# Optimization experiments

Hardware: AMD Instinct MI355X
Metric: run time of the kernel (lower is better)

The kernel has to match this reference:

```python
import jax, jax.numpy as jnp
import numpy as np
import math

E = 1024      # hidden_dim = embed_dim (num_heads=1 so head_dim=E)
ND = 512      # output_dim = asymmetric value dim
N_DOMAIN = 2048
LN_EPS = 1e-5
SCALE = math.sqrt(1.0 / E) * 2.0 * math.log(N_DOMAIN)


def layernorm(x, g, b):
    mu = jnp.mean(x, axis=-1, keepdims=True)
    var = jnp.var(x, axis=-1, keepdims=True)
    return (x - mu) * jax.lax.rsqrt(var + LN_EPS) * g + b


def setup_inputs() -> dict:
    key = jax.random.key(0)
    ks = jax.random.split(key, 5)
    B, L = 8, 2048
    return {
        "x": jax.random.normal(ks[0], (B, L, E), dtype=jnp.float32),
        "in_proj_w": jax.random.normal(ks[1], (2 * E + ND, E), dtype=jnp.float32) * 0.02,
        "w1": jax.random.normal(ks[2], (2048, ND), dtype=jnp.float32) * 0.02,
        "b1": jnp.zeros((2048,), dtype=jnp.float32),
        "w2": jax.random.normal(ks[3], (ND, 2048), dtype=jnp.float32) * 0.02,
        "b2": jnp.zeros((ND,), dtype=jnp.float32),
        "g1": jnp.ones((ND,), dtype=jnp.float32),
        "be1": jnp.zeros((ND,), dtype=jnp.float32),
        "g2": jnp.ones((ND,), dtype=jnp.float32),
        "be2": jnp.zeros((ND,), dtype=jnp.float32),
    }


def reference(x, in_proj_w, w1, b1, w2, b2, g1, be1, g2, be2):
    # fused in-projection (no bias): q,k get E dims, v gets ND dims
    proj = jnp.einsum("ble,fe->blf", x, in_proj_w)
    q = proj[..., :E]
    k = proj[..., E:2 * E]
    v = proj[..., 2 * E:]
    # custom scale: sqrt(1/head_dim) * 2 * log(N)
    scores = jnp.einsum("bld,bsd->bls", q * SCALE, k)  # [B, L, S]
    attn_w = jax.nn.softmax(scores, axis=-1)
    attn_out = jnp.einsum("bls,bsd->bld", attn_w, v)   # [B, L, ND] (no out proj)
    # skip=False (hidden_dim != output_dim): norm1(attn) only
    h = layernorm(attn_out, g1, be1)
    ff = jnp.einsum("bld,fd->blf", h, w1) + b1
    ff = jnp.einsum("blf,df->bld", jax.nn.relu(ff), w2) + b2
    return layernorm(h + ff, g2, be2)
```

## Files before the change

kernel.cpp:

```cpp
#include <hip/hip_runtime.h>
#include <hip/hip_bf16.h>

typedef unsigned short u16;
typedef unsigned int u32;
typedef float f32x4 __attribute__((ext_vector_type(4)));
typedef _Float16 f16x8 __attribute__((ext_vector_type(8)));
typedef u32 u32x4 __attribute__((ext_vector_type(4)));
typedef u32 u32x2 __attribute__((ext_vector_type(2)));

#define SEQ 2048
#define EDIM 1024

__device__ __forceinline__ u16 f2h(float f) {
  _Float16 h = (_Float16)f;
  return __builtin_bit_cast(u16, h);
}
__device__ __forceinline__ float h2f(u16 u) {
  return (float)__builtin_bit_cast(_Float16, u);
}
__device__ __forceinline__ u32 pk(float a, float b) {
  return (u32)f2h(a) | ((u32)f2h(b) << 16);
}

__global__ __launch_bounds__(256) void cvt_f16(const float* __restrict__ in,
                                               u16* __restrict__ out, int n8) {
  int i = blockIdx.x * 256 + threadIdx.x;
  if (i >= n8) return;
  const f32x4* p = (const f32x4*)(in + (size_t)i * 8);
  f32x4 a = p[0], b = p[1];
  u32x4 o = {pk(a[0], a[1]), pk(a[2], a[3]), pk(b[0], b[1]), pk(b[2], b[3])};
  *(u32x4*)(out + (size_t)i * 8) = o;
}

struct GemmP {
  const u16* A; const u16* B;
  int lda, ldb, K;
  long bsA, bsB, bsC;
  float* Cf;
  int ldc;
  u16* Cb;
  const float* bias;
  const u16* resid;
  u16* qk; u16* vT;
  float scale;
};

template <int EPI>
__global__ __launch_bounds__(256) void gemm_bt(GemmP p) {
  __shared__ __align__(16) char lds[32768];
  const int tid = threadIdx.x;
  const int lane = tid & 63;
  const int wave = tid >> 6;
  const int wm = wave >> 1, wn = wave & 1;
  const int bn0 = blockIdx.x * 128;
  const int bm0 = blockIdx.y * 128;
  const int z = blockIdx.z;

  const u16* gA[4]; const u16* gB[4];
  int ldsA[4], ldsB[4];
  {
    const u16* Ab = p.A + (long)z * p.bsA + (long)bm0 * p.lda;
    const u16* Bb = p.B + (long)z * p.bsB + (long)bn0 * p.ldb;
#pragma unroll
    for (int i = 0; i < 4; ++i) {
      int ch = i * 256 + tid;
      int row = ch >> 3, s = ch & 7;
      int ks = ((s ^ (row & 7)) << 3);
      gA[i] = Ab + (long)row * p.lda + ks;
      gB[i] = Bb + (long)row * p.ldb + ks;
      ldsA[i] = ch * 16;
      ldsB[i] = 16384 + ch * 16;
    }
  }
  auto stage = [&]() {
#pragma unroll
    for (int i = 0; i < 4; ++i) {
      __builtin_amdgcn_global_load_lds(
          (const __attribute__((address_space(1))) u32*)gA[i],
          (__attribute__((address_space(3))) u32*)(lds + ldsA[i]), 16, 0, 0);
      gA[i] += 64;
    }
#pragma unroll
    for (int i = 0; i < 4; ++i) {
      __builtin_amdgcn_global_load_lds(
          (const __attribute__((address_space(1))) u32*)gB[i],
          (__attribute__((address_space(3))) u32*)(lds + ldsB[i]), 16, 0, 0);
      gB[i] += 64;
    }
  };

  int ao[2][4], bo[2][4];
#pragma unroll
  for (int h = 0; h < 2; ++h) {
#pragma unroll
    for (int i = 0; i < 4; ++i) {
      int rA = wm * 64 + i * 16 + (lane & 15);
      ao[h][i] = rA * 128 + ((((h << 2) | (lane >> 4)) ^ (rA & 7)) << 4);
      int rB = wn * 64 + i * 16 + (lane & 15);
      bo[h][i] = 16384 + rB * 128 + ((((h << 2) | (lane >> 4)) ^ (rB & 7)) << 4);
    }
  }

  f32x4 acc[4][4] = {};
  stage();
  const int nk = p.K >> 6;
  for (int kt = 0; kt < nk; ++kt) {
    __syncthreads();
#pragma unroll
    for (int h = 0; h < 2; ++h) {
      f16x8 av[4], bv[4];
#pragma unroll
      for (int i = 0; i < 4; ++i) av[i] = *(const f16x8*)(lds + ao[h][i]);
#pragma unroll
      for (int j = 0; j < 4; ++j) bv[j] = *(const f16x8*)(lds + bo[h][j]);
#pragma unroll
      for (int i = 0; i < 4; ++i)
#pragma unroll
        for (int j = 0; j < 4; ++j)
          acc[i][j] = __builtin_amdgcn_mfma_f32_16x16x32_f16(av[i], bv[j], acc[i][j], 0, 0, 0);
    }
    __syncthreads();
    if (kt + 1 < nk) stage();
  }

#pragma unroll
  for (int i = 0; i < 4; ++i) {
#pragma unroll
    for (int j = 0; j < 4; ++j) {
      int mb = bm0 + wm * 64 + i * 16 + ((lane >> 4) << 2);
      int n = bn0 + wn * 64 + j * 16 + (lane & 15);
      if constexpr (EPI == 1) {
        int b = mb >> 11, l0 = mb & 2047;
        if (n < EDIM) {
          u16* dst = p.qk + (long)b * 4194304 + (long)l0 * 1024 + n;
#pragma unroll
          for (int r = 0; r < 4; ++r) dst[r * 1024] = f2h(acc[i][j][r] * p.scale);
        } else if (n < 2 * EDIM) {
          u16* dst = p.qk + (long)b * 4194304 + 2097152 + (long)l0 * 1024 + (n - EDIM);
#pragma unroll
          for (int r = 0; r < 4; ++r) dst[r * 1024] = f2h(acc[i][j][r]);
        } else {
          u16* dst = p.vT + (long)b * 1048576 + (long)(n - 2 * EDIM) * 2048 + l0;
          u32x2 w = {pk(acc[i][j][0], acc[i][j][1]), pk(acc[i][j][2], acc[i][j][3])};
          *(u32x2*)dst = w;
        }
      } else if constexpr (EPI == 2) {
        u16* dst = p.Cb + (long)mb * p.ldc + n;
        float bias = p.bias[n];
#pragma unroll
        for (int r = 0; r < 4; ++r) dst[(long)r * p.ldc] = f2h(fmaxf(acc[i][j][r] + bias, 0.f));
      } else if constexpr (EPI == 3) {
        float bias = p.bias[n];
        float* dst = p.Cf + (long)mb * 512 + n;
        const u16* rs = p.resid + (long)mb * 512 + n;
#pragma unroll
        for (int r = 0; r < 4; ++r) dst[r * 512] = acc[i][j][r] + bias + h2f(rs[r * 512]);
      } else {
        u16* dst = p.Cb + (long)z * p.bsC + (long)mb * p.ldc + n;
#pragma unroll
        for (int r = 0; r < 4; ++r) dst[(long)r * p.ldc] = f2h(acc[i][j][r]);
      }
    }
  }
}

__global__ __launch_bounds__(256) void softmax_rows(const u16* __restrict__ S,
                                                    u16* __restrict__ W, int b0) {
  int r = blockIdx.x;
  int z = r >> 11, l = r & 2047;
  int tid = threadIdx.x, lane = tid & 63, wv = tid >> 6;
  const u16* x = S + (long)r * 2048 + tid * 8;
  u32x4 raw = *(const u32x4*)x;
  float e[8];
#pragma unroll
  for (int q = 0; q < 4; ++q) {
    e[2 * q] = h2f((u16)(raw[q] & 0xffff));
    e[2 * q + 1] = h2f((u16)(raw[q] >> 16));
  }
  float m = e[0];
#pragma unroll
  for (int q = 1; q < 8; ++q) m = fmaxf(m, e[q]);
#pragma unroll
  for (int off = 32; off; off >>= 1) m = fmaxf(m, __shfl_xor(m, off));
  __shared__ float red[8];
  if (lane == 0) red[wv] = m;
  __syncthreads();
  m = fmaxf(fmaxf(red[0], red[1]), fmaxf(red[2], red[3]));
  float s = 0.f;
#pragma unroll
  for (int q = 0; q < 8; ++q) { e[q] = __expf(e[q] - m); s += e[q]; }
#pragma unroll
  for (int off = 32; off; off >>= 1) s += __shfl_xor(s, off);
  if (lane == 0) red[4 + wv] = s;
  __syncthreads();
  s = red[4] + red[5] + red[6] + red[7];
  float inv = 1.f / s;
  u32x4 o = {pk(e[0] * inv, e[1] * inv), pk(e[2] * inv, e[3] * inv),
             pk(e[4] * inv, e[5] * inv), pk(e[6] * inv, e[7] * inv)};
  *(u32x4*)(W + (long)(b0 + z) * 4194304 + (long)l * 2048 + tid * 8) = o;
}

template <int INF16, int OUTF16>
__global__ __launch_bounds__(256) void ln_rows(const void* __restrict__ X,
                                               const float* __restrict__ g,
                                               const float* __restrict__ bb,
                                               void* __restrict__ out) {
  int row = blockIdx.x * 4 + (threadIdx.x >> 6);
  int lane = threadIdx.x & 63;
  float v[8];
  if constexpr (INF16) {
    u32x4 raw = *(const u32x4*)((const u16*)X + (long)row * 512 + lane * 8);
#pragma unroll
    for (int q = 0; q < 4; ++q) {
      v[2 * q] = h2f((u16)(raw[q] & 0xffff));
      v[2 * q + 1] = h2f((u16)(raw[q] >> 16));
    }
  } else {
    const float* x = (const float*)X + (long)row * 512 + lane * 8;
    f32x4 a = *(const f32x4*)x, b = *(const f32x4*)(x + 4);
#pragma unroll
    for (int q = 0; q < 4; ++q) { v[q] = a[q]; v[4 + q] = b[q]; }
  }
  float s = 0.f, sq = 0.f;
#pragma unroll
  for (int q = 0; q < 8; ++q) { s += v[q]; sq += v[q] * v[q]; }
#pragma unroll
  for (int off = 32; off; off >>= 1) {
    s += __shfl_xor(s, off);
    sq += __shfl_xor(sq, off);
  }
  float mean = s * (1.f / 512.f);
  float var = sq * (1.f / 512.f) - mean * mean;
  float rstd = rsqrtf(var + 1e-5f);
  f32x4 g0 = *(const f32x4*)(g + lane * 8), g1v = *(const f32x4*)(g + lane * 8 + 4);
  f32x4 b0 = *(const f32x4*)(bb + lane * 8), b1v = *(const f32x4*)(bb + lane * 8 + 4);
  float o[8];
#pragma unroll
  for (int q = 0; q < 4; ++q) o[q] = (v[q] - mean) * rstd * g0[q] + b0[q];
#pragma unroll
  for (int q = 0; q < 4; ++q) o[4 + q] = (v[4 + q] - mean) * rstd * g1v[q] + b1v[q];
  if constexpr (OUTF16) {
    u32x4 pkd = {pk(o[0], o[1]), pk(o[2], o[3]), pk(o[4], o[5]), pk(o[6], o[7])};
    *(u32x4*)((u16*)out + (long)row * 512 + lane * 8) = pkd;
  } else {
    float* dst = (float*)out + (long)row * 512 + lane * 8;
    *(f32x4*)dst = (f32x4){o[0], o[1], o[2], o[3]};
    *(f32x4*)(dst + 4) = (f32x4){o[4], o[5], o[6], o[7]};
  }
}

extern "C" void kernel_launch(void* const* d_in, const int* in_sizes, int n_in,
                              void* d_out, int out_size, void* d_ws, size_t ws_size,
                              hipStream_t stream) {
  const float* x = (const float*)d_in[0];
  const float* wp = (const float*)d_in[1];
  const float* w1 = (const float*)d_in[2];
  const float* b1 = (const float*)d_in[3];
  const float* w2 = (const float*)d_in[4];
  const float* b2 = (const float*)d_in[5];
  const float* g1 = (const float*)d_in[6];
  const float* be1 = (const float*)d_in[7];
  const float* g2 = (const float*)d_in[8];
  const float* be2 = (const float*)d_in[9];

  char* ws = (char*)d_ws;
  size_t off = 0;
  auto alloc = [&](size_t bytes) {
    char* p = ws + off;
    off += (bytes + 255) & ~(size_t)255;
    return p;
  };
  u16* wpb = (u16*)alloc(2560 * 1024 * 2);
  u16* w1b = (u16*)alloc(2048 * 512 * 2);
  u16* w2b = (u16*)alloc(512 * 2048 * 2);
  char* xb_region = alloc(33554432);
  u16* qk = (u16*)alloc(67108864);
  u16* vT = (u16*)alloc(16777216);
  u16* hb = (u16*)alloc(16777216);
  char* sc_region = alloc(33554432);
  if (off > ws_size) return;

  u16* xb = (u16*)xb_region;
  u16* attn16 = (u16*)xb_region;
  u16* scores = (u16*)sc_region;
  float* y32 = (float*)sc_region;
  u16* ff1 = qk;

  const float SC = (float)(0.03125 * 2.0 * 7.6246189861593985);

  cvt_f16<<<dim3(8192), dim3(256), 0, stream>>>(x, xb, 2097152);
  cvt_f16<<<dim3(1280), dim3(256), 0, stream>>>(wp, wpb, 327680);
  cvt_f16<<<dim3(512), dim3(256), 0, stream>>>(w1, w1b, 131072);
  cvt_f16<<<dim3(512), dim3(256), 0, stream>>>(w2, w2b, 131072);

  {
    GemmP p{};
    p.A = xb; p.lda = 1024; p.B = wpb; p.ldb = 1024; p.K = 1024;
    p.qk = qk; p.vT = vT; p.scale = SC;
    gemm_bt<1><<<dim3(20, 128, 1), 256, 0, stream>>>(p);
  }

  for (int it = 0; it < 2; ++it) {
    int b0 = it * 4;
    GemmP p{};
    p.A = qk + (long)b0 * 4194304; p.lda = 1024; p.bsA = 4194304;
    p.B = qk + (long)b0 * 4194304 + 2097152; p.ldb = 1024; p.bsB = 4194304;
    p.K = 1024; p.Cb = scores; p.ldc = 2048; p.bsC = 4194304;
    gemm_bt<4><<<dim3(16, 16, 4), 256, 0, stream>>>(p);
    softmax_rows<<<dim3(8192), dim3(256), 0, stream>>>(scores, qk, b0);
  }

  {
    GemmP p{};
    p.A = qk; p.lda = 2048; p.bsA = 4194304;
    p.B = vT; p.ldb = 2048; p.bsB = 1048576;
    p.K = 2048; p.Cb = attn16; p.ldc = 512; p.bsC = 1048576;
    gemm_bt<4><<<dim3(4, 16, 8), 256, 0, stream>>>(p);
  }

  ln_rows<1, 1><<<dim3(4096), dim3(256), 0, stream>>>(attn16, g1, be1, hb);

  {
    GemmP p{};
    p.A = hb; p.lda = 512; p.B = w1b; p.ldb = 512; p.K = 512;
    p.Cb = ff1; p.ldc = 2048; p.bias = b1;
    gemm_bt<2><<<dim3(16, 128, 1), 256, 0, stream>>>(p);
  }

  {
    GemmP p{};
    p.A = ff1; p.lda = 2048; p.B = w2b; p.ldb = 2048; p.K = 2048;
    p.Cf = y32; p.bias = b2; p.resid = hb;
    gemm_bt<3><<<dim3(4, 128, 1), 256, 0, stream>>>(p);
  }

  ln_rows<0, 0><<<dim3(4096), dim3(256), 0, stream>>>(y32, g2, be2, (float*)d_out);
}
```

Measured before the change: 417.8 us.

## Merge conversion launches, batch all scores when workspace allows, store pre-LN sum in fp16

Replaces the four fp32-to-fp16 conversion launches with one kernel that dispatches on global index. The QK^T scores GEMM and softmax now cover all 8 batches in one pass when the workspace is large enough, falling back to two passes of 4 otherwise. The residual sum feeding the final layernorm is written as fp16 instead of fp32, halving that intermediate's traffic at some cost in precision. Together these cut launch count and memory traffic, but the larger scores buffer needs more workspace.

```diff
diff --git a/kernel.cpp b/kernel.cpp
--- a/kernel.cpp
+++ b/kernel.cpp
@@ -22,21 +22,31 @@
   return (u32)f2h(a) | ((u32)f2h(b) << 16);
 }
 
-__global__ __launch_bounds__(256) void cvt_f16(const float* __restrict__ in,
-                                               u16* __restrict__ out, int n8) {
+#define N_X  2097152
+#define N_WP 327680
+#define N_W1 131072
+#define N_W2 131072
+__global__ __launch_bounds__(256) void cvt_all(const float* __restrict__ x, u16* __restrict__ xb,
+                                               const float* __restrict__ wp, u16* __restrict__ wpb,
+                                               const float* __restrict__ w1, u16* __restrict__ w1b,
+                                               const float* __restrict__ w2, u16* __restrict__ w2b) {
   int i = blockIdx.x * 256 + threadIdx.x;
-  if (i >= n8) return;
-  const f32x4* p = (const f32x4*)(in + (size_t)i * 8);
+  const float* src; u16* dst; int li;
+  if (i < N_X) { src = x; dst = xb; li = i; }
+  else if (i < N_X + N_WP) { src = wp; dst = wpb; li = i - N_X; }
+  else if (i < N_X + N_WP + N_W1) { src = w1; dst = w1b; li = i - N_X - N_WP; }
+  else if (i < N_X + N_WP + N_W1 + N_W2) { src = w2; dst = w2b; li = i - N_X - N_WP - N_W1; }
+  else return;
+  const f32x4* p = (const f32x4*)(src + (size_t)li * 8);
   f32x4 a = p[0], b = p[1];
   u32x4 o = {pk(a[0], a[1]), pk(a[2], a[3]), pk(b[0], b[1]), pk(b[2], b[3])};
-  *(u32x4*)(out + (size_t)i * 8) = o;
+  *(u32x4*)(dst + (size_t)li * 8) = o;
 }
 
 struct GemmP {
   const u16* A; const u16* B;
   int lda, ldb, K;
   long bsA, bsB, bsC;
-  float* Cf;
   int ldc;
   u16* Cb;
   const float* bias;
@@ -151,10 +161,10 @@
         for (int r = 0; r < 4; ++r) dst[(long)r * p.ldc] = f2h(fmaxf(acc[i][j][r] + bias, 0.f));
       } else if constexpr (EPI == 3) {
         float bias = p.bias[n];
-        float* dst = p.Cf + (long)mb * 512 + n;
+        u16* dst = p.Cb + (long)mb * 512 + n;
         const u16* rs = p.resid + (long)mb * 512 + n;
 #pragma unroll
-        for (int r = 0; r < 4; ++r) dst[r * 512] = acc[i][j][r] + bias + h2f(rs[r * 512]);
+        for (int r = 0; r < 4; ++r) dst[r * 512] = f2h(acc[i][j][r] + bias + h2f(rs[r * 512]));
       } else {
         u16* dst = p.Cb + (long)z * p.bsC + (long)mb * p.ldc + n;
 #pragma unroll
@@ -277,21 +287,19 @@
   u16* qk = (u16*)alloc(67108864);
   u16* vT = (u16*)alloc(16777216);
   u16* hb = (u16*)alloc(16777216);
-  char* sc_region = alloc(33554432);
+  int bpl = (ws_size >= off + (size_t)67108864) ? 8 : 4;
+  char* sc_region = alloc((size_t)bpl * 2048 * 2048 * 2);
   if (off > ws_size) return;
 
   u16* xb = (u16*)xb_region;
   u16* attn16 = (u16*)xb_region;
   u16* scores = (u16*)sc_region;
-  float* y32 = (float*)sc_region;
+  u16* y16 = (u16*)sc_region;
   u16* ff1 = qk;
 
   const float SC = (float)(0.03125 * 2.0 * 7.6246189861593985);
 
-  cvt_f16<<<dim3(8192), dim3(256), 0, stream>>>(x, xb, 2097152);
-  cvt_f16<<<dim3(1280), dim3(256), 0, stream>>>(wp, wpb, 327680);
-  cvt_f16<<<dim3(512), dim3(256), 0, stream>>>(w1, w1b, 131072);
-  cvt_f16<<<dim3(512), dim3(256), 0, stream>>>(w2, w2b, 131072);
+  cvt_all<<<dim3(10496), dim3(256), 0, stream>>>(x, xb, wp, wpb, w1, w1b, w2, w2b);
 
   {
     GemmP p{};
@@ -300,14 +308,14 @@
     gemm_bt<1><<<dim3(20, 128, 1), 256, 0, stream>>>(p);
   }
 
-  for (int it = 0; it < 2; ++it) {
-    int b0 = it * 4;
+  for (int it = 0; it < 8 / bpl; ++it) {
+    int b0 = it * bpl;
     GemmP p{};
     p.A = qk + (long)b0 * 4194304; p.lda = 1024; p.bsA = 4194304;
     p.B = qk + (long)b0 * 4194304 + 2097152; p.ldb = 1024; p.bsB = 4194304;
     p.K = 1024; p.Cb = scores; p.ldc = 2048; p.bsC = 4194304;
-    gemm_bt<4><<<dim3(16, 16, 4), 256, 0, stream>>>(p);
-    softmax_rows<<<dim3(8192), dim3(256), 0, stream>>>(scores, qk, b0);
+    gemm_bt<4><<<dim3(16, 16, bpl), 256, 0, stream>>>(p);
+    softmax_rows<<<dim3(bpl * 2048), dim3(256), 0, stream>>>(scores, qk, b0);
   }
 
   {
@@ -330,9 +338,9 @@
   {
     GemmP p{};
     p.A = ff1; p.lda = 2048; p.B = w2b; p.ldb = 2048; p.K = 2048;
-    p.Cf = y32; p.bias = b2; p.resid = hb;
+    p.Cb = y16; p.bias = b2; p.resid = hb;
     gemm_bt<3><<<dim3(4, 128, 1), 256, 0, stream>>>(p);
   }
 
-  ln_rows<0, 0><<<dim3(4096), dim3(256), 0, stream>>>(y32, g2, be2, (float*)d_out);
-}
+  ln_rows<1, 0><<<dim3(4096), dim3(256), 0, stream>>>(y16, g2, be2, (float*)d_out);
+}
```

New measurement: 400.1 us. -4.2%, faster.
